# Optimization experiments

Measured on AMD Instinct MI355X. Metric: run time of the kernel, lower is better.

The kernel has to match this reference:

```python
import jax, jax.numpy as jnp
import numpy as np

NUM_HEADS = 4
NUM_GROUPS = 8
EPS = 1e-5


def group_norm(x, gamma, beta):
    B, C, H, W = x.shape
    xg = x.reshape(B, NUM_GROUPS, C // NUM_GROUPS, H, W)
    mean = xg.mean(axis=(2, 3, 4), keepdims=True)
    var = xg.var(axis=(2, 3, 4), keepdims=True)
    xn = ((xg - mean) * jax.lax.rsqrt(var + EPS)).reshape(B, C, H, W)
    return xn * gamma[None, :, None, None] + beta[None, :, None, None]


def setup_inputs() -> dict:
    key = jax.random.key(0)
    k1, k2, k3 = jax.random.split(key, 3)
    B, C, H, W = 16, 512, 32, 32
    x = jax.random.normal(k1, (B, C, H, W), dtype=jnp.float32)
    gn_gamma = jnp.ones((C,), dtype=jnp.float32)
    gn_beta = jnp.zeros((C,), dtype=jnp.float32)
    w_qkv = jax.random.normal(k2, (3 * C, C), dtype=jnp.float32) * 0.02
    w_proj = jax.random.normal(k3, (C, C), dtype=jnp.float32) * 0.02
    b_proj = jnp.zeros((C,), dtype=jnp.float32)
    return {"x": x, "gn_gamma": gn_gamma, "gn_beta": gn_beta,
            "w_qkv": w_qkv, "w_proj": w_proj, "b_proj": b_proj}


def reference(x, gn_gamma, gn_beta, w_qkv, w_proj, b_proj):
    B, C, H, W = x.shape
    nh = NUM_HEADS
    hd = C // nh
    N = H * W

    x_norm = group_norm(x, gn_gamma, gn_beta)
    # 1x1 conv == channel matmul: (B,C,H,W) x (3C,C) -> (B,3C,H,W)
    qkv = jnp.einsum('bchw,dc->bdhw', x_norm, w_qkv)
    qkv = qkv.reshape(B, 3, nh, hd, N)
    q, k, v = qkv[:, 0], qkv[:, 1], qkv[:, 2]  # each (B, nh, hd, N)

    scale = hd ** (-0.5)
    attn = jnp.einsum('bhci,bhcj->bhij', q, k) * scale  # (B, nh, N, N)
    attn = jax.nn.softmax(attn, axis=-1)
    out = jnp.einsum('bhij,bhcj->bhci', attn, v)  # (B, nh, hd, N)
    out = out.reshape(B, C, H, W)

    proj = jnp.einsum('bchw,dc->bdhw', out, w_proj) + b_proj[None, :, None, None]
    return x + proj
```

## Files before the change

### kernel.cpp

```cpp
#include <hip/hip_runtime.h>
#include <stdint.h>

typedef unsigned short u16;
typedef unsigned int u32;
typedef __attribute__((ext_vector_type(8))) short short8;
typedef __attribute__((ext_vector_type(4))) float f32x4;
typedef __attribute__((ext_vector_type(16))) float f32x16;
typedef __attribute__((ext_vector_type(4))) u32 u32x4;

#define BATCH 16
#define CCH   512
#define NPIX  1024
#define NGRP  8
#define CPG   64
#define NHEAD 4
#define HDIM  128

__device__ __forceinline__ u16 f2bf(float f) {
  union { float f; u32 u; } v; v.f = f;
  u32 u = v.u;
  u32 r = (u + 0x7FFFu + ((u >> 16) & 1u)) >> 16;
  return (u16)r;
}

__device__ __forceinline__ void gload16(const void* g, void* l) {
  typedef __attribute__((address_space(3))) u32 L;
  typedef __attribute__((address_space(1))) const u32 G;
  __builtin_amdgcn_global_load_lds((G*)(uintptr_t)g, (L*)(u32)(uintptr_t)l, 16, 0, 0);
}

#define CVTPK(dst, a, b) asm("v_cvt_pk_bf16_f32 %0, %1, %2" : "=v"(dst) : "v"(a), "v"(b))
#define PLSWAP(a, b) asm("v_permlane32_swap_b32 %0, %1" : "+v"(a), "+v"(b))

__device__ __forceinline__ short8 rd512(const char* base, int r, int ck, int hi) {
  int byte = ((r >> 2) * 512) +
             ((((r & 3) * 128) + ck * 32 + hi * 16) ^ (((r >> 2) & 15) << 4));
  return *reinterpret_cast<const short8*>(base + byte);
}

__device__ __forceinline__ float softmax_pack(const f32x16& s0, const f32x16& s1, short8* pf) {
  float ps[4] = {0.f, 0.f, 0.f, 0.f};
  u32 pw[16];
  #pragma unroll
  for (int u = 0; u < 8; ++u) {
    float pa = exp2f(s0[2*u]);  float pb = exp2f(s0[2*u+1]);
    float pc = exp2f(s1[2*u]);  float pd = exp2f(s1[2*u+1]);
    ps[u & 3] += (pa + pb) + (pc + pd);
    CVTPK(pw[u],     pa, pb);
    CVTPK(pw[8 + u], pc, pd);
  }
  PLSWAP(pw[0], pw[2]);  PLSWAP(pw[1], pw[3]);
  PLSWAP(pw[4], pw[6]);  PLSWAP(pw[5], pw[7]);
  PLSWAP(pw[8], pw[10]); PLSWAP(pw[9], pw[11]);
  PLSWAP(pw[12], pw[14]); PLSWAP(pw[13], pw[15]);
  #pragma unroll
  for (int f = 0; f < 4; ++f) {
    u32x4 t = {pw[f*4], pw[f*4+1], pw[f*4+2], pw[f*4+3]};
    pf[f] = __builtin_bit_cast(short8, t);
  }
  float psum = (ps[0] + ps[1]) + (ps[2] + ps[3]);
  psum += __shfl_xor(psum, 32);
  return psum;
}

__global__ void gn_stats_k(const float* __restrict__ x, float* __restrict__ part) {
  int bg = blockIdx.x >> 3, sl = blockIdx.x & 7;
  const float* p = x + (size_t)bg * (CPG * NPIX) + sl * 8192;
  float s = 0.f, ss = 0.f;
  for (int i = threadIdx.x; i < 2048; i += 256) {
    float4 v = reinterpret_cast<const float4*>(p)[i];
    s  += v.x + v.y + v.z + v.w;
    ss += v.x*v.x + v.y*v.y + v.z*v.z + v.w*v.w;
  }
  for (int o = 32; o > 0; o >>= 1) { s += __shfl_down(s, o); ss += __shfl_down(ss, o); }
  __shared__ float sh[8];
  int wid = threadIdx.x >> 6;
  if ((threadIdx.x & 63) == 0) { sh[wid*2] = s; sh[wid*2+1] = ss; }
  __syncthreads();
  if (threadIdx.x == 0) {
    part[blockIdx.x*2]   = sh[0]+sh[2]+sh[4]+sh[6];
    part[blockIdx.x*2+1] = sh[1]+sh[3]+sh[5]+sh[7];
  }
}

__global__ __launch_bounds__(256) void gn_apply_t(const float* __restrict__ x,
                                                  const float* __restrict__ gamma,
                                                  const float* __restrict__ beta,
                                                  const float* __restrict__ part,
                                                  u16* __restrict__ xnT) {
  const int p0 = blockIdx.x * 64;
  const int c0 = blockIdx.y * 64;
  const int b  = blockIdx.z;
  __shared__ float lt[64][66];

  const int bg = b * NGRP + (c0 >> 6);
  float s = 0.f, ss = 0.f;
  #pragma unroll
  for (int k2 = 0; k2 < 8; ++k2) { s += part[(bg*8 + k2)*2]; ss += part[(bg*8 + k2)*2 + 1]; }
  const float invn = 1.f / (float)(CPG * NPIX);
  const float mean = s * invn;
  const float rstd = rsqrtf(ss * invn - mean * mean + 1e-5f);

  const int t = threadIdx.x;
  #pragma unroll
  for (int pass = 0; pass < 4; ++pass) {
    int c   = c0 + (t >> 4) + pass * 16;
    int pix = p0 + (t & 15) * 4;
    float ga = gamma[c] * rstd;
    float be = beta[c] - mean * ga;
    float4 v = *reinterpret_cast<const float4*>(&x[((size_t)(b*CCH + c)) * NPIX + pix]);
    int pl = (t & 15) * 4, cl = (t >> 4) + pass * 16;
    lt[pl+0][cl] = v.x*ga + be;
    lt[pl+1][cl] = v.y*ga + be;
    lt[pl+2][cl] = v.z*ga + be;
    lt[pl+3][cl] = v.w*ga + be;
  }
  __syncthreads();
  const int pl = t >> 2, cq = (t & 3) * 16;
  u32 wbuf[8];
  #pragma unroll
  for (int e = 0; e < 8; ++e) {
    u16 lo = f2bf(lt[pl][cq + e*2]);
    u16 hi = f2bf(lt[pl][cq + e*2 + 1]);
    wbuf[e] = (u32)lo | ((u32)hi << 16);
  }
  u32* dst = (u32*)&xnT[((size_t)(b*NPIX + p0 + pl)) * CCH + c0 + cq];
  #pragma unroll
  for (int e = 0; e < 8; ++e) dst[e] = wbuf[e];
}

__global__ void f2bf_all(const float* __restrict__ wqkv, const float* __restrict__ wproj,
                         u16* __restrict__ wq, u16* __restrict__ wp, float qs) {
  int i = blockIdx.x * 256 + threadIdx.x;
  float4 v; u16* dst; float sc = 1.f;
  if (i < 196608) {
    v = reinterpret_cast<const float4*>(wqkv)[i];
    if (i < 65536) sc = qs;
    dst = wq + (size_t)i * 4;
  } else {
    v = reinterpret_cast<const float4*>(wproj)[i - 196608];
    dst = wp + (size_t)(i - 196608) * 4;
  }
  u32 lo = (u32)f2bf(v.x*sc) | ((u32)f2bf(v.y*sc) << 16);
  u32 hi = (u32)f2bf(v.z*sc) | ((u32)f2bf(v.w*sc) << 16);
  *reinterpret_cast<uint2*>(dst) = make_uint2(lo, hi);
}

__global__ __launch_bounds__(256, 2) void gemm_qkv(const u16* __restrict__ xnT,
                                                   const u16* __restrict__ wq_bf,
                                                   u16* __restrict__ outQ,
                                                   u16* __restrict__ outK,
                                                   u16* __restrict__ outV) {
  __shared__ __align__(16) char smem[65536];

  const int id = blockIdx.x;
  const int wg = (id & 7) * 192 + (id >> 3);
  const bool mode0 = (wg < 1024);
  int rt, ct;
  if (mode0) { rt = wg >> 3; ct = wg & 7; }
  else       { int w1 = wg - 1024; rt = w1 & 3; ct = w1 >> 2; }

  const char* Ab = mode0 ? (const char*)xnT + (size_t)rt * 131072
                         : (const char*)wq_bf + (size_t)(8 + rt) * 131072;
  const char* Bb = mode0 ? (const char*)wq_bf + (size_t)ct * 131072
                         : (const char*)xnT + (size_t)ct * 131072;

  const int t = threadIdx.x;
  const int lane = t & 63, w = t >> 6;
  const int q = lane & 31, hi = lane >> 5;
  const int rh = (w >> 1) * 64, ch = (w & 1) * 64;

  int soff[4];
  #pragma unroll
  for (int i = 0; i < 4; ++i) {
    int p = w*4096 + i*1024 + lane*16;
    int lrow = p >> 9, off = p & 511;
    int loff = off ^ ((lrow & 15) << 4);
    soff[i] = (lrow*4 + (loff >> 7)) * 1024 + (loff & 127);
  }

  #pragma unroll
  for (int i = 0; i < 4; ++i) {
    gload16(Ab + soff[i], smem +         w*4096 + i*1024);
    gload16(Bb + soff[i], smem + 16384 + w*4096 + i*1024);
  }

  f32x16 acc[2][2] = {};

  for (int kt = 0; kt < 8; ++kt) {
    asm volatile("s_waitcnt vmcnt(0)" ::: "memory");
    __syncthreads();
    const char* cur = smem + (kt & 1) * 32768;
    if (kt + 1 < 8) {
      char* nxt = smem + ((kt + 1) & 1) * 32768;
      #pragma unroll
      for (int i = 0; i < 4; ++i) {
        gload16(Ab + (kt+1)*128 + soff[i], nxt +         w*4096 + i*1024);
        gload16(Bb + (kt+1)*128 + soff[i], nxt + 16384 + w*4096 + i*1024);
      }
    }
    __builtin_amdgcn_s_setprio(1);
    #pragma unroll
    for (int ck = 0; ck < 4; ++ck) {
      short8 af0 = rd512(cur,         rh + q,      ck, hi);
      short8 af1 = rd512(cur,         rh + 32 + q, ck, hi);
      short8 bf0 = rd512(cur + 16384, ch + q,      ck, hi);
      short8 bf1 = rd512(cur + 16384, ch + 32 + q, ck, hi);
      acc[0][0] = __builtin_amdgcn_mfma_f32_32x32x16_bf16(af0, bf0, acc[0][0], 0, 0, 0);
      acc[0][1] = __builtin_amdgcn_mfma_f32_32x32x16_bf16(af0, bf1, acc[0][1], 0, 0, 0);
      acc[1][0] = __builtin_amdgcn_mfma_f32_32x32x16_bf16(af1, bf0, acc[1][0], 0, 0, 0);
      acc[1][1] = __builtin_amdgcn_mfma_f32_32x32x16_bf16(af1, bf1, acc[1][1], 0, 0, 0);
    }
    __builtin_amdgcn_s_setprio(0);
  }

  __syncthreads();
  u16* Dt = (u16*)smem;
  #pragma unroll
  for (int r = 0; r < 16; ++r) {
    int ar = (r & 3) + 8*(r >> 2) + 4*hi;
    Dt[(rh +      ar) * 136 + ch +      q] = f2bf(acc[0][0][r]);
    Dt[(rh +      ar) * 136 + ch + 32 + q] = f2bf(acc[0][1][r]);
    Dt[(rh + 32 + ar) * 136 + ch +      q] = f2bf(acc[1][0][r]);
    Dt[(rh + 32 + ar) * 136 + ch + 32 + q] = f2bf(acc[1][1][r]);
  }
  __syncthreads();

  const int rl = t >> 1, hoff = (t & 1) * 64;
  uint4 buf[8];
  const uint4* s4 = reinterpret_cast<const uint4*>(&Dt[rl*136 + hoff]);
  #pragma unroll
  for (int e = 0; e < 8; ++e) buf[e] = s4[e];

  u16* gdst;
  if (mode0) {
    const int tok0 = rt * 128;
    const int b = tok0 >> 10, pix0 = tok0 & 1023;
    const int h = ct & 3;
    u16* base = (ct >= 4) ? outK : outQ;
    gdst = base + ((size_t)((b*NHEAD + h)) * NPIX + pix0 + rl) * HDIM + hoff;
  } else {
    const int m0 = rt * 128, tok0 = ct * 128;
    const int b = tok0 >> 10, pix0 = tok0 & 1023;
    gdst = outV + ((size_t)(b*CCH + m0 + rl)) * NPIX + pix0 + hoff;
  }
  uint4* g4 = reinterpret_cast<uint4*>(gdst);
  #pragma unroll
  for (int e = 0; e < 8; ++e) g4[e] = buf[e];
}

__global__ __launch_bounds__(256, 2) void gemm_proj(const u16* __restrict__ wp_bf,
                                                    const u16* __restrict__ attnO,
                                                    const float* __restrict__ xres,
                                                    const float* __restrict__ bias,
                                                    float* __restrict__ outF) {
  __shared__ __align__(16) char smem[65536];

  const int id = blockIdx.x;
  const int wg = (id & 7) * 64 + (id >> 3);
  const int rt = wg & 3, ct = wg >> 2;

  const char* Ab = (const char*)wp_bf + (size_t)rt * 131072;
  const char* Bb = (const char*)attnO + (size_t)ct * 131072;

  const int t = threadIdx.x;
  const int lane = t & 63, w = t >> 6;
  const int q = lane & 31, hi = lane >> 5;
  const int rh = (w >> 1) * 64, ch = (w & 1) * 64;

  int soff[4];
  #pragma unroll
  for (int i = 0; i < 4; ++i) {
    int p = w*4096 + i*1024 + lane*16;
    int lrow = p >> 9, off = p & 511;
    int loff = off ^ ((lrow & 15) << 4);
    soff[i] = (lrow*4 + (loff >> 7)) * 1024 + (loff & 127);
  }

  #pragma unroll
  for (int i = 0; i < 4; ++i) {
    gload16(Ab + soff[i], smem +         w*4096 + i*1024);
    gload16(Bb + soff[i], smem + 16384 + w*4096 + i*1024);
  }

  f32x16 acc[2][2] = {};

  for (int kt = 0; kt < 8; ++kt) {
    asm volatile("s_waitcnt vmcnt(0)" ::: "memory");
    __syncthreads();
    const char* cur = smem + (kt & 1) * 32768;
    if (kt + 1 < 8) {
      char* nxt = smem + ((kt + 1) & 1) * 32768;
      #pragma unroll
      for (int i = 0; i < 4; ++i) {
        gload16(Ab + (kt+1)*128 + soff[i], nxt +         w*4096 + i*1024);
        gload16(Bb + (kt+1)*128 + soff[i], nxt + 16384 + w*4096 + i*1024);
      }
    }
    __builtin_amdgcn_s_setprio(1);
    #pragma unroll
    for (int ck = 0; ck < 4; ++ck) {
      short8 af0 = rd512(cur,         rh + q,      ck, hi);
      short8 af1 = rd512(cur,         rh + 32 + q, ck, hi);
      short8 bf0 = rd512(cur + 16384, ch + q,      ck, hi);
      short8 bf1 = rd512(cur + 16384, ch + 32 + q, ck, hi);
      acc[0][0] = __builtin_amdgcn_mfma_f32_32x32x16_bf16(af0, bf0, acc[0][0], 0, 0, 0);
      acc[0][1] = __builtin_amdgcn_mfma_f32_32x32x16_bf16(af0, bf1, acc[0][1], 0, 0, 0);
      acc[1][0] = __builtin_amdgcn_mfma_f32_32x32x16_bf16(af1, bf0, acc[1][0], 0, 0, 0);
      acc[1][1] = __builtin_amdgcn_mfma_f32_32x32x16_bf16(af1, bf1, acc[1][1], 0, 0, 0);
    }
    __builtin_amdgcn_s_setprio(0);
  }

  const int m0 = rt * 128, tok0 = ct * 128;
  const int b = tok0 >> 10, pix0 = tok0 & 1023;
  #pragma unroll
  for (int r = 0; r < 16; ++r) {
    int ar = (r & 3) + 8*(r >> 2) + 4*hi;
    int m0r = m0 + rh + ar, m1r = m0 + rh + 32 + ar;
    size_t o00 = ((size_t)(b*CCH + m0r)) * NPIX + pix0 + ch + q;
    size_t o01 = o00 + 32;
    size_t o10 = ((size_t)(b*CCH + m1r)) * NPIX + pix0 + ch + q;
    size_t o11 = o10 + 32;
    outF[o00] = xres[o00] + acc[0][0][r] + bias[m0r];
    outF[o01] = xres[o01] + acc[0][1][r] + bias[m0r];
    outF[o10] = xres[o10] + acc[1][0][r] + bias[m1r];
    outF[o11] = xres[o11] + acc[1][1][r] + bias[m1r];
  }
}

__global__ __launch_bounds__(256, 2) void attn_k(const u16* __restrict__ Qt,
                                                 const u16* __restrict__ Kt,
                                                 const u16* __restrict__ Vb,
                                                 u16* __restrict__ attnO) {
  int id = blockIdx.x;
  int swz = (id & 7) * 64 + (id >> 3);
  const int qt = swz & 7;
  const int h  = (swz >> 3) & 3;
  const int b  = swz >> 5;
  const int bh = b * NHEAD + h;

  __shared__ __align__(16) char smem[65536];

  const int t = threadIdx.x;
  const int lane = t & 63, w = t >> 6;
  const int q = lane & 31, hi = lane >> 5;

  const u16*  Qb    = Qt + ((size_t)bh * NPIX + qt*128 + w*32 + q) * HDIM;
  const char* Kbase = (const char*)(Kt + (size_t)bh * NPIX * HDIM);
  const char* Vbase = (const char*)(Vb + ((size_t)b*CCH + h*HDIM) * NPIX);

  short8 qf[8];
  #pragma unroll
  for (int ck = 0; ck < 8; ++ck)
    qf[ck] = *reinterpret_cast<const short8*>(&Qb[ck*16 + hi*8]);

  int koff[4], voff[4];
  #pragma unroll
  for (int i = 0; i < 4; ++i) {
    int d = w*4096 + i*1024 + lane*16;
    int r = d >> 8, cb = d & 255;
    int col = cb ^ ((r & 15) << 4);
    koff[i] = r*256 + col;
    int half = col >> 7, kvb = col & 127;
    voff[i] = (2*r + half)*2048 + kvb;
  }

  const int ksw = (q & 15) << 4;
  const int vsw = (q >> 1) << 4;

  f32x16 of[4] = {};
  float l_run = 0.f;
  short8 pf[4];

  #pragma unroll
  for (int i = 0; i < 4; ++i)
    gload16(Kbase + koff[i],                  smem +         w*4096 + i*1024);
  #pragma unroll
  for (int i = 0; i < 4; ++i)
    gload16(Kbase + (size_t)64*256 + koff[i], smem + 16384 + w*4096 + i*1024);
  #pragma unroll
  for (int i = 0; i < 4; ++i)
    gload16(Vbase + voff[i],                  smem + 32768 + w*4096 + i*1024);
  asm volatile("s_waitcnt vmcnt(0)" ::: "memory");
  __syncthreads();

  {
    f32x16 sn[2] = {};
    #pragma unroll
    for (int ck = 0; ck < 8; ++ck) {
      const short8 kf0 = *reinterpret_cast<const short8*>(smem + q*256      + ((ck*32 + hi*16) ^ ksw));
      const short8 kf1 = *reinterpret_cast<const short8*>(smem + (32+q)*256 + ((ck*32 + hi*16) ^ ksw));
      sn[0] = __builtin_amdgcn_mfma_f32_32x32x16_bf16(kf0, qf[ck], sn[0], 0, 0, 0);
      sn[1] = __builtin_amdgcn_mfma_f32_32x32x16_bf16(kf1, qf[ck], sn[1], 0, 0, 0);
    }
    l_run += softmax_pack(sn[0], sn[1], pf);
  }

  for (int tt = 0; tt < 16; ++tt) {
    asm volatile("s_waitcnt vmcnt(4)" ::: "memory");
    __builtin_amdgcn_s_barrier();

    const char* kcur = smem + (((tt+1) & 1) << 14);
    const char* vcur = smem + 32768 + ((tt & 1) << 14);

    if (tt + 2 < 16) {
      char* kdst = smem + ((tt & 1) << 14);
      #pragma unroll
      for (int i = 0; i < 4; ++i)
        gload16(Kbase + (size_t)(tt+2)*64*256 + koff[i], kdst + w*4096 + i*1024);
    }
    if (tt + 1 < 16) {
      char* vdst = smem + 32768 + (((tt+1) & 1) << 14);
      #pragma unroll
      for (int i = 0; i < 4; ++i)
        gload16(Vbase + (size_t)(tt+1)*128 + voff[i], vdst + w*4096 + i*1024);
    }

    f32x16 sn[2] = {};
    __builtin_amdgcn_s_setprio(1);
    if (tt + 1 < 16) {
      #pragma unroll
      for (int ck = 0; ck < 8; ++ck) {
        const short8 kf0 = *reinterpret_cast<const short8*>(kcur + q*256      + ((ck*32 + hi*16) ^ ksw));
        const short8 kf1 = *reinterpret_cast<const short8*>(kcur + (32+q)*256 + ((ck*32 + hi*16) ^ ksw));
        sn[0] = __builtin_amdgcn_mfma_f32_32x32x16_bf16(kf0, qf[ck], sn[0], 0, 0, 0);
        sn[1] = __builtin_amdgcn_mfma_f32_32x32x16_bf16(kf1, qf[ck], sn[1], 0, 0, 0);
      }
    }
    __builtin_amdgcn_s_setprio(0);

    if (tt < 14)       asm volatile("s_waitcnt vmcnt(8)" ::: "memory");
    else if (tt == 14) asm volatile("s_waitcnt vmcnt(4)" ::: "memory");
    else               asm volatile("s_waitcnt vmcnt(0)" ::: "memory");
    __builtin_amdgcn_s_barrier();

    __builtin_amdgcn_s_setprio(1);
    #pragma unroll
    for (int cg = 0; cg < 4; ++cg) {
      const char* vrow = vcur + (cg*16 + (q >> 1))*256;
      const int hb = (q & 1) << 7;
      #pragma unroll
      for (int kc = 0; kc < 4; ++kc)
        of[cg] = __builtin_amdgcn_mfma_f32_32x32x16_bf16(
            *reinterpret_cast<const short8*>(vrow + ((hb + kc*32 + hi*16) ^ vsw)),
            pf[kc], of[cg], 0, 0, 0);
    }
    __builtin_amdgcn_s_setprio(0);

    if (tt + 1 < 16)
      l_run += softmax_pack(sn[0], sn[1], pf);
  }

  float inv = 1.f / l_run;
  u16* orow = attnO + ((size_t)(b*NPIX + qt*128 + w*32 + q)) * CCH + h*HDIM;
  #pragma unroll
  for (int cg = 0; cg < 4; ++cg) {
    #pragma unroll
    for (int u = 0; u < 8; ++u) {
      int c = cg*32 + ((2*u) & 3) + 8*(u >> 1) + 4*hi;
      u32 pk = (u32)f2bf(of[cg][2*u] * inv) | ((u32)f2bf(of[cg][2*u+1] * inv) << 16);
      *reinterpret_cast<u32*>(&orow[c]) = pk;
    }
  }
}

extern "C" void kernel_launch(void* const* d_in, const int* in_sizes, int n_in,
                              void* d_out, int out_size, void* d_ws, size_t ws_size,
                              hipStream_t stream) {
  const float* x     = (const float*)d_in[0];
  const float* gamma = (const float*)d_in[1];
  const float* beta  = (const float*)d_in[2];
  const float* wqkv  = (const float*)d_in[3];
  const float* wproj = (const float*)d_in[4];
  const float* bproj = (const float*)d_in[5];
  float* out = (float*)d_out;

  char* ws = (char*)d_ws;
  float* part   = (float*)ws;
  u16*   xnT    = (u16*)(ws + 8192);
  u16*   wq_bf  = (u16*)(ws + 8192 + (16u<<20));
  u16*   wp_bf  = (u16*)((char*)wq_bf + 1572864);
  u16*   Qt     = (u16*)((char*)wp_bf + 524288);
  u16*   Kt     = (u16*)((char*)Qt + (16u<<20));
  u16*   Vb     = (u16*)((char*)Kt + (16u<<20));
  u16*   attnO  = (u16*)((char*)Vb + (16u<<20));

  const float qs = 0.08838834764831845f * 1.44269504088896f;

  gn_stats_k<<<dim3(1024), dim3(256), 0, stream>>>(x, part);
  gn_apply_t<<<dim3(16, 8, BATCH), dim3(256), 0, stream>>>(x, gamma, beta, part, xnT);
  f2bf_all<<<dim3(1024), dim3(256), 0, stream>>>(wqkv, wproj, wq_bf, wp_bf, qs);

  gemm_qkv<<<dim3(1536), dim3(256), 0, stream>>>(xnT, wq_bf, Qt, Kt, Vb);

  attn_k<<<dim3(512), dim3(256), 0, stream>>>(Qt, Kt, Vb, attnO);

  gemm_proj<<<dim3(512), dim3(256), 0, stream>>>(wp_bf, attnO, x, bproj, out);
}
```

Measured before the change: 122.5 us.

## Split KV tile across wave pairs with two query subtiles per wave in attention

```diff
diff --git a/kernel.cpp b/kernel.cpp
--- a/kernel.cpp
+++ b/kernel.cpp
@@ -38,29 +38,23 @@
   return *reinterpret_cast<const short8*>(base + byte);
 }
 
-__device__ __forceinline__ float softmax_pack(const f32x16& s0, const f32x16& s1, short8* pf) {
-  float ps[4] = {0.f, 0.f, 0.f, 0.f};
-  u32 pw[16];
+__device__ __forceinline__ float softmax_pack32(const f32x16& sn, short8* pf) {
+  float ps = 0.f;
+  u32 pw[8];
   #pragma unroll
   for (int u = 0; u < 8; ++u) {
-    float pa = exp2f(s0[2*u]);  float pb = exp2f(s0[2*u+1]);
-    float pc = exp2f(s1[2*u]);  float pd = exp2f(s1[2*u+1]);
-    ps[u & 3] += (pa + pb) + (pc + pd);
-    CVTPK(pw[u],     pa, pb);
-    CVTPK(pw[8 + u], pc, pd);
-  }
-  PLSWAP(pw[0], pw[2]);  PLSWAP(pw[1], pw[3]);
-  PLSWAP(pw[4], pw[6]);  PLSWAP(pw[5], pw[7]);
-  PLSWAP(pw[8], pw[10]); PLSWAP(pw[9], pw[11]);
-  PLSWAP(pw[12], pw[14]); PLSWAP(pw[13], pw[15]);
-  #pragma unroll
-  for (int f = 0; f < 4; ++f) {
-    u32x4 t = {pw[f*4], pw[f*4+1], pw[f*4+2], pw[f*4+3]};
-    pf[f] = __builtin_bit_cast(short8, t);
-  }
-  float psum = (ps[0] + ps[1]) + (ps[2] + ps[3]);
-  psum += __shfl_xor(psum, 32);
-  return psum;
+    float pa = exp2f(sn[2*u]);
+    float pb = exp2f(sn[2*u+1]);
+    ps += pa + pb;
+    CVTPK(pw[u], pa, pb);
+  }
+  PLSWAP(pw[0], pw[2]); PLSWAP(pw[1], pw[3]);
+  PLSWAP(pw[4], pw[6]); PLSWAP(pw[5], pw[7]);
+  u32x4 t0 = {pw[0], pw[1], pw[2], pw[3]};
+  u32x4 t1 = {pw[4], pw[5], pw[6], pw[7]};
+  pf[0] = __builtin_bit_cast(short8, t0);
+  pf[1] = __builtin_bit_cast(short8, t1);
+  return ps;
 }
 
 __global__ void gn_stats_k(const float* __restrict__ x, float* __restrict__ part) {
@@ -340,20 +334,23 @@
   const int b  = swz >> 5;
   const int bh = b * NHEAD + h;
 
-  __shared__ __align__(16) char smem[65536];
+  __shared__ __align__(16) char smem[66048];
 
   const int t = threadIdx.x;
   const int lane = t & 63, w = t >> 6;
   const int q = lane & 31, hi = lane >> 5;
-
-  const u16*  Qb    = Qt + ((size_t)bh * NPIX + qt*128 + w*32 + q) * HDIM;
+  const int qsub = w & 1, kvh = w >> 1;
+
+  const u16*  Qb    = Qt + ((size_t)bh * NPIX + qt*128 + qsub*64 + q) * HDIM;
   const char* Kbase = (const char*)(Kt + (size_t)bh * NPIX * HDIM);
   const char* Vbase = (const char*)(Vb + ((size_t)b*CCH + h*HDIM) * NPIX);
 
-  short8 qf[8];
-  #pragma unroll
-  for (int ck = 0; ck < 8; ++ck)
-    qf[ck] = *reinterpret_cast<const short8*>(&Qb[ck*16 + hi*8]);
+  short8 qf0[8], qf1[8];
+  #pragma unroll
+  for (int ck = 0; ck < 8; ++ck) {
+    qf0[ck] = *reinterpret_cast<const short8*>(&Qb[ck*16 + hi*8]);
+    qf1[ck] = *reinterpret_cast<const short8*>(&Qb[(size_t)32*HDIM + ck*16 + hi*8]);
+  }
 
   int koff[4], voff[4];
   #pragma unroll
@@ -366,74 +363,53 @@
     voff[i] = (2*r + half)*2048 + kvb;
   }
 
-  const int ksw = (q & 15) << 4;
-  const int vsw = (q >> 1) << 4;
-
-  f32x16 of[4] = {};
-  float l_run = 0.f;
-  short8 pf[4];
+  const int ksw  = (q & 15) << 4;
+  const int vsw  = (q >> 1) << 4;
+  const int krow = (kvh*32 + q) * 256;
+  const int vkvb = kvh * 64;
+
+  f32x16 of0[4] = {};
+  f32x16 of1[4] = {};
+  float l0 = 0.f, l1 = 0.f;
 
   #pragma unroll
   for (int i = 0; i < 4; ++i)
-    gload16(Kbase + koff[i],                  smem +         w*4096 + i*1024);
+    gload16(Kbase + koff[i], smem + w*4096 + i*1024);
   #pragma unroll
   for (int i = 0; i < 4; ++i)
-    gload16(Kbase + (size_t)64*256 + koff[i], smem + 16384 + w*4096 + i*1024);
-  #pragma unroll
-  for (int i = 0; i < 4; ++i)
-    gload16(Vbase + voff[i],                  smem + 32768 + w*4096 + i*1024);
-  asm volatile("s_waitcnt vmcnt(0)" ::: "memory");
-  __syncthreads();
-
-  {
-    f32x16 sn[2] = {};
+    gload16(Vbase + voff[i], smem + 32768 + w*4096 + i*1024);
+
+  for (int tt = 0; tt < 16; ++tt) {
+    asm volatile("s_waitcnt vmcnt(0)" ::: "memory");
+    __builtin_amdgcn_s_barrier();
+
+    const char* kcur = smem + ((tt & 1) << 14);
+    const char* vcur = smem + 32768 + ((tt & 1) << 14);
+
+    if (tt + 1 < 16) {
+      char* kd = smem + (((tt+1) & 1) << 14);
+      char* vd = smem + 32768 + (((tt+1) & 1) << 14);
+      #pragma unroll
+      for (int i = 0; i < 4; ++i)
+        gload16(Kbase + (size_t)(tt+1)*16384 + koff[i], kd + w*4096 + i*1024);
+      #pragma unroll
+      for (int i = 0; i < 4; ++i)
+        gload16(Vbase + (size_t)(tt+1)*128 + voff[i], vd + w*4096 + i*1024);
+    }
+
+    f32x16 sn0 = {}, sn1 = {};
+    __builtin_amdgcn_s_setprio(1);
     #pragma unroll
     for (int ck = 0; ck < 8; ++ck) {
-      const short8 kf0 = *reinterpret_cast<const short8*>(smem + q*256      + ((ck*32 + hi*16) ^ ksw));
-      const short8 kf1 = *reinterpret_cast<const short8*>(smem + (32+q)*256 + ((ck*32 + hi*16) ^ ksw));
-      sn[0] = __builtin_amdgcn_mfma_f32_32x32x16_bf16(kf0, qf[ck], sn[0], 0, 0, 0);
-      sn[1] = __builtin_amdgcn_mfma_f32_32x32x16_bf16(kf1, qf[ck], sn[1], 0, 0, 0);
-    }
-    l_run += softmax_pack(sn[0], sn[1], pf);
-  }
-
-  for (int tt = 0; tt < 16; ++tt) {
-    asm volatile("s_waitcnt vmcnt(4)" ::: "memory");
-    __builtin_amdgcn_s_barrier();
-
-    const char* kcur = smem + (((tt+1) & 1) << 14);
-    const char* vcur = smem + 32768 + ((tt & 1) << 14);
-
-    if (tt + 2 < 16) {
-      char* kdst = smem + ((tt & 1) << 14);
-      #pragma unroll
-      for (int i = 0; i < 4; ++i)
-        gload16(Kbase + (size_t)(tt+2)*64*256 + koff[i], kdst + w*4096 + i*1024);
-    }
-    if (tt + 1 < 16) {
-      char* vdst = smem + 32768 + (((tt+1) & 1) << 14);
-      #pragma unroll
-      for (int i = 0; i < 4; ++i)
-        gload16(Vbase + (size_t)(tt+1)*128 + voff[i], vdst + w*4096 + i*1024);
-    }
-
-    f32x16 sn[2] = {};
-    __builtin_amdgcn_s_setprio(1);
-    if (tt + 1 < 16) {
-      #pragma unroll
-      for (int ck = 0; ck < 8; ++ck) {
-        const short8 kf0 = *reinterpret_cast<const short8*>(kcur + q*256      + ((ck*32 + hi*16) ^ ksw));
-        const short8 kf1 = *reinterpret_cast<const short8*>(kcur + (32+q)*256 + ((ck*32 + hi*16) ^ ksw));
-        sn[0] = __builtin_amdgcn_mfma_f32_32x32x16_bf16(kf0, qf[ck], sn[0], 0, 0, 0);
-        sn[1] = __builtin_amdgcn_mfma_f32_32x32x16_bf16(kf1, qf[ck], sn[1], 0, 0, 0);
-      }
+      const short8 kf = *reinterpret_cast<const short8*>(kcur + krow + ((ck*32 + hi*16) ^ ksw));
+      sn0 = __builtin_amdgcn_mfma_f32_32x32x16_bf16(kf, qf0[ck], sn0, 0, 0, 0);
+      sn1 = __builtin_amdgcn_mfma_f32_32x32x16_bf16(kf, qf1[ck], sn1, 0, 0, 0);
     }
     __builtin_amdgcn_s_setprio(0);
 
-    if (tt < 14)       asm volatile("s_waitcnt vmcnt(8)" ::: "memory");
-    else if (tt == 14) asm volatile("s_waitcnt vmcnt(4)" ::: "memory");
-    else               asm volatile("s_waitcnt vmcnt(0)" ::: "memory");
-    __builtin_amdgcn_s_barrier();
+    short8 pfa[2], pfb[2];
+    l0 += softmax_pack32(sn0, pfa);
+    l1 += softmax_pack32(sn1, pfb);
 
     __builtin_amdgcn_s_setprio(1);
     #pragma unroll
@@ -441,26 +417,54 @@
       const char* vrow = vcur + (cg*16 + (q >> 1))*256;
       const int hb = (q & 1) << 7;
       #pragma unroll
-      for (int kc = 0; kc < 4; ++kc)
-        of[cg] = __builtin_amdgcn_mfma_f32_32x32x16_bf16(
-            *reinterpret_cast<const short8*>(vrow + ((hb + kc*32 + hi*16) ^ vsw)),
-            pf[kc], of[cg], 0, 0, 0);
+      for (int kc = 0; kc < 2; ++kc) {
+        const short8 vf = *reinterpret_cast<const short8*>(
+            vrow + ((hb + vkvb + kc*32 + hi*16) ^ vsw));
+        of0[cg] = __builtin_amdgcn_mfma_f32_32x32x16_bf16(vf, pfa[kc], of0[cg], 0, 0, 0);
+        of1[cg] = __builtin_amdgcn_mfma_f32_32x32x16_bf16(vf, pfb[kc], of1[cg], 0, 0, 0);
+      }
     }
     __builtin_amdgcn_s_setprio(0);
-
-    if (tt + 1 < 16)
-      l_run += softmax_pack(sn[0], sn[1], pf);
-  }
-
-  float inv = 1.f / l_run;
-  u16* orow = attnO + ((size_t)(b*NPIX + qt*128 + w*32 + q)) * CCH + h*HDIM;
-  #pragma unroll
-  for (int cg = 0; cg < 4; ++cg) {
+  }
+
+  __syncthreads();
+  float* exf = (float*)smem;
+  float* exl = (float*)(smem + 65536);
+
+  l0 += __shfl_xor(l0, 32);
+  l1 += __shfl_xor(l1, 32);
+
+  if (kvh == 1) {
     #pragma unroll
-    for (int u = 0; u < 8; ++u) {
-      int c = cg*32 + ((2*u) & 3) + 8*(u >> 1) + 4*hi;
-      u32 pk = (u32)f2bf(of[cg][2*u] * inv) | ((u32)f2bf(of[cg][2*u+1] * inv) << 16);
-      *reinterpret_cast<u32*>(&orow[c]) = pk;
+    for (int cg = 0; cg < 4; ++cg)
+      #pragma unroll
+      for (int r = 0; r < 16; ++r) {
+        exf[qsub*8192 + cg*2048 + r*128 +      lane] = of0[cg][r];
+        exf[qsub*8192 + cg*2048 + r*128 + 64 + lane] = of1[cg][r];
+      }
+    if (lane < 32) {
+      exl[qsub*64 +      q] = l0;
+      exl[qsub*64 + 32 + q] = l1;
+    }
+  }
+  __syncthreads();
+  if (kvh == 0) {
+    const float inv0 = 1.f / (l0 + exl[qsub*64 + q]);
+    const float inv1 = 1.f / (l1 + exl[qsub*64 + 32 + q]);
+    u16* orow0 = attnO + ((size_t)(b*NPIX + qt*128 + qsub*64 + q)) * CCH + h*HDIM;
+    u16* orow1 = orow0 + (size_t)32 * CCH;
+    #pragma unroll
+    for (int cg = 0; cg < 4; ++cg) {
+      #pragma unroll
+      for (int u = 0; u < 8; ++u) {
+        int c = cg*32 + ((2*u) & 3) + 8*(u >> 1) + 4*hi;
+        float a0 = (of0[cg][2*u]   + exf[qsub*8192 + cg*2048 + (2*u)*128 +      lane]) * inv0;
+        float a1 = (of0[cg][2*u+1] + exf[qsub*8192 + cg*2048 + (2*u+1)*128 +    lane]) * inv0;
+        float b0 = (of1[cg][2*u]   + exf[qsub*8192 + cg*2048 + (2*u)*128 + 64 + lane]) * inv1;
+        float b1 = (of1[cg][2*u+1] + exf[qsub*8192 + cg*2048 + (2*u+1)*128 + 64 + lane]) * inv1;
+        *reinterpret_cast<u32*>(&orow0[c]) = (u32)f2bf(a0) | ((u32)f2bf(a1) << 16);
+        *reinterpret_cast<u32*>(&orow1[c]) = (u32)f2bf(b0) | ((u32)f2bf(b1) << 16);
+      }
     }
   }
 }
```

New measurement: 142.0 us. 15.9% more time.

## Switch attention Q/K/V and probabilities to FP8 MFMA

Applied to the files above, without the earlier changes.

```diff
diff --git a/kernel.cpp b/kernel.cpp
--- a/kernel.cpp
+++ b/kernel.cpp
@@ -1,8 +1,10 @@
 #include <hip/hip_runtime.h>
 #include <stdint.h>
 
+typedef unsigned char u8;
 typedef unsigned short u16;
 typedef unsigned int u32;
+typedef long long i64;
 typedef __attribute__((ext_vector_type(8))) short short8;
 typedef __attribute__((ext_vector_type(4))) float f32x4;
 typedef __attribute__((ext_vector_type(16))) float f32x16;
@@ -22,6 +24,14 @@
   u32 r = (u + 0x7FFFu + ((u >> 16) & 1u)) >> 16;
   return (u16)r;
 }
+__device__ __forceinline__ u8 f2fp8(float f) {
+  return (u8)(__builtin_amdgcn_cvt_pk_fp8_f32(f, 0.f, 0, false) & 0xff);
+}
+__device__ __forceinline__ u32 pack4_fp8(float a, float b, float c, float d) {
+  u32 w = (u32)__builtin_amdgcn_cvt_pk_fp8_f32(a, b, 0, false);
+  w = (u32)__builtin_amdgcn_cvt_pk_fp8_f32(c, d, (int)w, true);
+  return w;
+}
 
 __device__ __forceinline__ void gload16(const void* g, void* l) {
   typedef __attribute__((address_space(3))) u32 L;
@@ -29,38 +39,12 @@
   __builtin_amdgcn_global_load_lds((G*)(uintptr_t)g, (L*)(u32)(uintptr_t)l, 16, 0, 0);
 }
 
-#define CVTPK(dst, a, b) asm("v_cvt_pk_bf16_f32 %0, %1, %2" : "=v"(dst) : "v"(a), "v"(b))
 #define PLSWAP(a, b) asm("v_permlane32_swap_b32 %0, %1" : "+v"(a), "+v"(b))
 
 __device__ __forceinline__ short8 rd512(const char* base, int r, int ck, int hi) {
   int byte = ((r >> 2) * 512) +
              ((((r & 3) * 128) + ck * 32 + hi * 16) ^ (((r >> 2) & 15) << 4));
   return *reinterpret_cast<const short8*>(base + byte);
-}
-
-__device__ __forceinline__ float softmax_pack(const f32x16& s0, const f32x16& s1, short8* pf) {
-  float ps[4] = {0.f, 0.f, 0.f, 0.f};
-  u32 pw[16];
-  #pragma unroll
-  for (int u = 0; u < 8; ++u) {
-    float pa = exp2f(s0[2*u]);  float pb = exp2f(s0[2*u+1]);
-    float pc = exp2f(s1[2*u]);  float pd = exp2f(s1[2*u+1]);
-    ps[u & 3] += (pa + pb) + (pc + pd);
-    CVTPK(pw[u],     pa, pb);
-    CVTPK(pw[8 + u], pc, pd);
-  }
-  PLSWAP(pw[0], pw[2]);  PLSWAP(pw[1], pw[3]);
-  PLSWAP(pw[4], pw[6]);  PLSWAP(pw[5], pw[7]);
-  PLSWAP(pw[8], pw[10]); PLSWAP(pw[9], pw[11]);
-  PLSWAP(pw[12], pw[14]); PLSWAP(pw[13], pw[15]);
-  #pragma unroll
-  for (int f = 0; f < 4; ++f) {
-    u32x4 t = {pw[f*4], pw[f*4+1], pw[f*4+2], pw[f*4+3]};
-    pf[f] = __builtin_bit_cast(short8, t);
-  }
-  float psum = (ps[0] + ps[1]) + (ps[2] + ps[3]);
-  psum += __shfl_xor(psum, 32);
-  return psum;
 }
 
 __global__ void gn_stats_k(const float* __restrict__ x, float* __restrict__ part) {
@@ -130,27 +114,26 @@
 }
 
 __global__ void f2bf_all(const float* __restrict__ wqkv, const float* __restrict__ wproj,
-                         u16* __restrict__ wq, u16* __restrict__ wp, float qs) {
+                         u16* __restrict__ wq, u16* __restrict__ wp) {
   int i = blockIdx.x * 256 + threadIdx.x;
-  float4 v; u16* dst; float sc = 1.f;
+  float4 v; u16* dst;
   if (i < 196608) {
     v = reinterpret_cast<const float4*>(wqkv)[i];
-    if (i < 65536) sc = qs;
     dst = wq + (size_t)i * 4;
   } else {
     v = reinterpret_cast<const float4*>(wproj)[i - 196608];
     dst = wp + (size_t)(i - 196608) * 4;
   }
-  u32 lo = (u32)f2bf(v.x*sc) | ((u32)f2bf(v.y*sc) << 16);
-  u32 hi = (u32)f2bf(v.z*sc) | ((u32)f2bf(v.w*sc) << 16);
+  u32 lo = (u32)f2bf(v.x) | ((u32)f2bf(v.y) << 16);
+  u32 hi = (u32)f2bf(v.z) | ((u32)f2bf(v.w) << 16);
   *reinterpret_cast<uint2*>(dst) = make_uint2(lo, hi);
 }
 
 __global__ __launch_bounds__(256, 2) void gemm_qkv(const u16* __restrict__ xnT,
                                                    const u16* __restrict__ wq_bf,
-                                                   u16* __restrict__ outQ,
-                                                   u16* __restrict__ outK,
-                                                   u16* __restrict__ outV) {
+                                                   u8* __restrict__ outQ,
+                                                   u8* __restrict__ outK,
+                                                   u8* __restrict__ outV) {
   __shared__ __align__(16) char smem[65536];
 
   const int id = blockIdx.x;
@@ -215,29 +198,29 @@
   }
 
   __syncthreads();
-  u16* Dt = (u16*)smem;
+  u8* Dt = (u8*)smem;
   #pragma unroll
   for (int r = 0; r < 16; ++r) {
     int ar = (r & 3) + 8*(r >> 2) + 4*hi;
-    Dt[(rh +      ar) * 136 + ch +      q] = f2bf(acc[0][0][r]);
-    Dt[(rh +      ar) * 136 + ch + 32 + q] = f2bf(acc[0][1][r]);
-    Dt[(rh + 32 + ar) * 136 + ch +      q] = f2bf(acc[1][0][r]);
-    Dt[(rh + 32 + ar) * 136 + ch + 32 + q] = f2bf(acc[1][1][r]);
+    Dt[(rh +      ar) * 144 + ch +      q] = f2fp8(acc[0][0][r]);
+    Dt[(rh +      ar) * 144 + ch + 32 + q] = f2fp8(acc[0][1][r]);
+    Dt[(rh + 32 + ar) * 144 + ch +      q] = f2fp8(acc[1][0][r]);
+    Dt[(rh + 32 + ar) * 144 + ch + 32 + q] = f2fp8(acc[1][1][r]);
   }
   __syncthreads();
 
   const int rl = t >> 1, hoff = (t & 1) * 64;
-  uint4 buf[8];
-  const uint4* s4 = reinterpret_cast<const uint4*>(&Dt[rl*136 + hoff]);
-  #pragma unroll
-  for (int e = 0; e < 8; ++e) buf[e] = s4[e];
-
-  u16* gdst;
+  uint4 buf[4];
+  const uint4* s4 = reinterpret_cast<const uint4*>(&Dt[rl*144 + hoff]);
+  #pragma unroll
+  for (int e = 0; e < 4; ++e) buf[e] = s4[e];
+
+  u8* gdst;
   if (mode0) {
     const int tok0 = rt * 128;
     const int b = tok0 >> 10, pix0 = tok0 & 1023;
     const int h = ct & 3;
-    u16* base = (ct >= 4) ? outK : outQ;
+    u8* base = (ct >= 4) ? outK : outQ;
     gdst = base + ((size_t)((b*NHEAD + h)) * NPIX + pix0 + rl) * HDIM + hoff;
   } else {
     const int m0 = rt * 128, tok0 = ct * 128;
@@ -246,7 +229,7 @@
   }
   uint4* g4 = reinterpret_cast<uint4*>(gdst);
   #pragma unroll
-  for (int e = 0; e < 8; ++e) g4[e] = buf[e];
+  for (int e = 0; e < 4; ++e) g4[e] = buf[e];
 }
 
 __global__ __launch_bounds__(256, 2) void gemm_proj(const u16* __restrict__ wp_bf,
@@ -329,9 +312,9 @@
   }
 }
 
-__global__ __launch_bounds__(256, 2) void attn_k(const u16* __restrict__ Qt,
-                                                 const u16* __restrict__ Kt,
-                                                 const u16* __restrict__ Vb,
+__global__ __launch_bounds__(256, 2) void attn_k(const u8* __restrict__ Qt,
+                                                 const u8* __restrict__ Kt,
+                                                 const u8* __restrict__ Vb,
                                                  u16* __restrict__ attnO) {
   int id = blockIdx.x;
   int swz = (id & 7) * 64 + (id >> 3);
@@ -340,116 +323,151 @@
   const int b  = swz >> 5;
   const int bh = b * NHEAD + h;
 
-  __shared__ __align__(16) char smem[65536];
+  __shared__ __align__(16) char smem[32768];
 
   const int t = threadIdx.x;
   const int lane = t & 63, w = t >> 6;
   const int q = lane & 31, hi = lane >> 5;
 
-  const u16*  Qb    = Qt + ((size_t)bh * NPIX + qt*128 + w*32 + q) * HDIM;
-  const char* Kbase = (const char*)(Kt + (size_t)bh * NPIX * HDIM);
-  const char* Vbase = (const char*)(Vb + ((size_t)b*CCH + h*HDIM) * NPIX);
-
-  short8 qf[8];
+  const u8*   Qb    = Qt + ((size_t)bh * NPIX + qt*128 + w*32 + q) * HDIM;
+  const char* Kbase = (const char*)Kt + (size_t)bh * NPIX * HDIM;
+  const char* Vbase = (const char*)Vb + ((size_t)b*CCH + h*HDIM) * NPIX;
+
+  i64 qf[8];
   #pragma unroll
   for (int ck = 0; ck < 8; ++ck)
-    qf[ck] = *reinterpret_cast<const short8*>(&Qb[ck*16 + hi*8]);
-
-  int koff[4], voff[4];
-  #pragma unroll
-  for (int i = 0; i < 4; ++i) {
-    int d = w*4096 + i*1024 + lane*16;
-    int r = d >> 8, cb = d & 255;
-    int col = cb ^ ((r & 15) << 4);
-    koff[i] = r*256 + col;
-    int half = col >> 7, kvb = col & 127;
-    voff[i] = (2*r + half)*2048 + kvb;
-  }
-
-  const int ksw = (q & 15) << 4;
-  const int vsw = (q >> 1) << 4;
+    qf[ck] = *reinterpret_cast<const i64*>(Qb + ck*16 + hi*8);
+
+  int koff[2], voff[2];
+  #pragma unroll
+  for (int i = 0; i < 2; ++i) {
+    int d = i*4096 + w*1024 + lane*16;
+    int r = d >> 7, x = d & 127;
+    koff[i] = r*128 + (x ^ ((r & 15) << 3));
+    int vc = 2*r + (x >> 6);
+    voff[i] = vc*1024 + ((x & 63) ^ ((r & 7) << 3));
+  }
+
+  const int ksw = (q & 15) << 3;
 
   f32x16 of[4] = {};
   float l_run = 0.f;
-  short8 pf[4];
-
-  #pragma unroll
-  for (int i = 0; i < 4; ++i)
-    gload16(Kbase + koff[i],                  smem +         w*4096 + i*1024);
-  #pragma unroll
-  for (int i = 0; i < 4; ++i)
-    gload16(Kbase + (size_t)64*256 + koff[i], smem + 16384 + w*4096 + i*1024);
-  #pragma unroll
-  for (int i = 0; i < 4; ++i)
-    gload16(Vbase + voff[i],                  smem + 32768 + w*4096 + i*1024);
+  i64 pf[4];
+  const float qs2 = 0.08838834764831845f * 1.44269504088896f;
+
+  #pragma unroll
+  for (int i = 0; i < 2; ++i)
+    gload16(Kbase + koff[i],        smem +        i*4096 + w*1024);
+  #pragma unroll
+  for (int i = 0; i < 2; ++i)
+    gload16(Kbase + 8192 + koff[i], smem + 8192 + i*4096 + w*1024);
+  #pragma unroll
+  for (int i = 0; i < 2; ++i)
+    gload16(Vbase + voff[i],        smem + 16384 + i*4096 + w*1024);
   asm volatile("s_waitcnt vmcnt(0)" ::: "memory");
   __syncthreads();
 
   {
-    f32x16 sn[2] = {};
+    f32x16 sn0 = {}, sn1 = {};
     #pragma unroll
     for (int ck = 0; ck < 8; ++ck) {
-      const short8 kf0 = *reinterpret_cast<const short8*>(smem + q*256      + ((ck*32 + hi*16) ^ ksw));
-      const short8 kf1 = *reinterpret_cast<const short8*>(smem + (32+q)*256 + ((ck*32 + hi*16) ^ ksw));
-      sn[0] = __builtin_amdgcn_mfma_f32_32x32x16_bf16(kf0, qf[ck], sn[0], 0, 0, 0);
-      sn[1] = __builtin_amdgcn_mfma_f32_32x32x16_bf16(kf1, qf[ck], sn[1], 0, 0, 0);
-    }
-    l_run += softmax_pack(sn[0], sn[1], pf);
+      const i64 kf0 = *reinterpret_cast<const i64*>(smem + q*128      + ((ck*16 + hi*8) ^ ksw));
+      const i64 kf1 = *reinterpret_cast<const i64*>(smem + (32+q)*128 + ((ck*16 + hi*8) ^ ksw));
+      sn0 = __builtin_amdgcn_mfma_f32_32x32x16_fp8_fp8(kf0, qf[ck], sn0, 0, 0, 0);
+      sn1 = __builtin_amdgcn_mfma_f32_32x32x16_fp8_fp8(kf1, qf[ck], sn1, 0, 0, 0);
+    }
+    float ps = 0.f;
+    float p[16];
+    #pragma unroll
+    for (int g = 0; g < 2; ++g) {
+      const f32x16& sn = g ? sn1 : sn0;
+      #pragma unroll
+      for (int r = 0; r < 16; ++r) { p[r] = exp2f(sn[r] * qs2); ps += p[r]; }
+      u32 pkl0 = pack4_fp8(p[0], p[1], p[2], p[3]);
+      u32 pkh0 = pack4_fp8(p[4], p[5], p[6], p[7]);
+      u32 pkl1 = pack4_fp8(p[8], p[9], p[10], p[11]);
+      u32 pkh1 = pack4_fp8(p[12], p[13], p[14], p[15]);
+      PLSWAP(pkl0, pkh0);
+      PLSWAP(pkl1, pkh1);
+      pf[g*2]   = (i64)(((unsigned long long)pkh0 << 32) | pkl0);
+      pf[g*2+1] = (i64)(((unsigned long long)pkh1 << 32) | pkl1);
+    }
+    ps += __shfl_xor(ps, 32);
+    l_run += ps;
   }
 
   for (int tt = 0; tt < 16; ++tt) {
-    asm volatile("s_waitcnt vmcnt(4)" ::: "memory");
+    asm volatile("s_waitcnt vmcnt(2)" ::: "memory");
     __builtin_amdgcn_s_barrier();
 
-    const char* kcur = smem + (((tt+1) & 1) << 14);
-    const char* vcur = smem + 32768 + ((tt & 1) << 14);
+    const char* kcur = smem + (((tt+1) & 1) << 13);
+    const char* vcur = smem + 16384 + ((tt & 1) << 13);
 
     if (tt + 2 < 16) {
-      char* kdst = smem + ((tt & 1) << 14);
-      #pragma unroll
-      for (int i = 0; i < 4; ++i)
-        gload16(Kbase + (size_t)(tt+2)*64*256 + koff[i], kdst + w*4096 + i*1024);
+      char* kd = smem + ((tt & 1) << 13);
+      #pragma unroll
+      for (int i = 0; i < 2; ++i)
+        gload16(Kbase + (size_t)(tt+2)*8192 + koff[i], kd + i*4096 + w*1024);
     }
     if (tt + 1 < 16) {
-      char* vdst = smem + 32768 + (((tt+1) & 1) << 14);
-      #pragma unroll
-      for (int i = 0; i < 4; ++i)
-        gload16(Vbase + (size_t)(tt+1)*128 + voff[i], vdst + w*4096 + i*1024);
-    }
-
-    f32x16 sn[2] = {};
+      char* vd = smem + 16384 + (((tt+1) & 1) << 13);
+      #pragma unroll
+      for (int i = 0; i < 2; ++i)
+        gload16(Vbase + (size_t)(tt+1)*64 + voff[i], vd + i*4096 + w*1024);
+    }
+
+    f32x16 sn0 = {}, sn1 = {};
     __builtin_amdgcn_s_setprio(1);
     if (tt + 1 < 16) {
       #pragma unroll
       for (int ck = 0; ck < 8; ++ck) {
-        const short8 kf0 = *reinterpret_cast<const short8*>(kcur + q*256      + ((ck*32 + hi*16) ^ ksw));
-        const short8 kf1 = *reinterpret_cast<const short8*>(kcur + (32+q)*256 + ((ck*32 + hi*16) ^ ksw));
-        sn[0] = __builtin_amdgcn_mfma_f32_32x32x16_bf16(kf0, qf[ck], sn[0], 0, 0, 0);
-        sn[1] = __builtin_amdgcn_mfma_f32_32x32x16_bf16(kf1, qf[ck], sn[1], 0, 0, 0);
+        const i64 kf0 = *reinterpret_cast<const i64*>(kcur + q*128      + ((ck*16 + hi*8) ^ ksw));
+        const i64 kf1 = *reinterpret_cast<const i64*>(kcur + (32+q)*128 + ((ck*16 + hi*8) ^ ksw));
+        sn0 = __builtin_amdgcn_mfma_f32_32x32x16_fp8_fp8(kf0, qf[ck], sn0, 0, 0, 0);
+        sn1 = __builtin_amdgcn_mfma_f32_32x32x16_fp8_fp8(kf1, qf[ck], sn1, 0, 0, 0);
       }
     }
     __builtin_amdgcn_s_setprio(0);
 
-    if (tt < 14)       asm volatile("s_waitcnt vmcnt(8)" ::: "memory");
-    else if (tt == 14) asm volatile("s_waitcnt vmcnt(4)" ::: "memory");
+    if (tt < 14)       asm volatile("s_waitcnt vmcnt(4)" ::: "memory");
+    else if (tt == 14) asm volatile("s_waitcnt vmcnt(2)" ::: "memory");
     else               asm volatile("s_waitcnt vmcnt(0)" ::: "memory");
     __builtin_amdgcn_s_barrier();
 
     __builtin_amdgcn_s_setprio(1);
     #pragma unroll
     for (int cg = 0; cg < 4; ++cg) {
-      const char* vrow = vcur + (cg*16 + (q >> 1))*256;
-      const int hb = (q & 1) << 7;
-      #pragma unroll
-      for (int kc = 0; kc < 4; ++kc)
-        of[cg] = __builtin_amdgcn_mfma_f32_32x32x16_bf16(
-            *reinterpret_cast<const short8*>(vrow + ((hb + kc*32 + hi*16) ^ vsw)),
-            pf[kc], of[cg], 0, 0, 0);
+      const int c = cg*32 + q;
+      const char* vrow = vcur + (c >> 1)*128 + (c & 1)*64;
+      const int vsw = ((c >> 1) & 7) << 3;
+      #pragma unroll
+      for (int kc = 0; kc < 4; ++kc) {
+        const i64 vf = *reinterpret_cast<const i64*>(vrow + ((kc*16 + hi*8) ^ vsw));
+        of[cg] = __builtin_amdgcn_mfma_f32_32x32x16_fp8_fp8(vf, pf[kc], of[cg], 0, 0, 0);
+      }
     }
     __builtin_amdgcn_s_setprio(0);
 
-    if (tt + 1 < 16)
-      l_run += softmax_pack(sn[0], sn[1], pf);
+    if (tt + 1 < 16) {
+      float ps = 0.f;
+      float p[16];
+      #pragma unroll
+      for (int g = 0; g < 2; ++g) {
+        const f32x16& sn = g ? sn1 : sn0;
+        #pragma unroll
+        for (int r = 0; r < 16; ++r) { p[r] = exp2f(sn[r] * qs2); ps += p[r]; }
+        u32 pkl0 = pack4_fp8(p[0], p[1], p[2], p[3]);
+        u32 pkh0 = pack4_fp8(p[4], p[5], p[6], p[7]);
+        u32 pkl1 = pack4_fp8(p[8], p[9], p[10], p[11]);
+        u32 pkh1 = pack4_fp8(p[12], p[13], p[14], p[15]);
+        PLSWAP(pkl0, pkh0);
+        PLSWAP(pkl1, pkh1);
+        pf[g*2]   = (i64)(((unsigned long long)pkh0 << 32) | pkl0);
+        pf[g*2+1] = (i64)(((unsigned long long)pkh1 << 32) | pkl1);
+      }
+      ps += __shfl_xor(ps, 32);
+      l_run += ps;
+    }
   }
 
   float inv = 1.f / l_run;
@@ -481,16 +499,14 @@
   u16*   xnT    = (u16*)(ws + 8192);
   u16*   wq_bf  = (u16*)(ws + 8192 + (16u<<20));
   u16*   wp_bf  = (u16*)((char*)wq_bf + 1572864);
-  u16*   Qt     = (u16*)((char*)wp_bf + 524288);
-  u16*   Kt     = (u16*)((char*)Qt + (16u<<20));
-  u16*   Vb     = (u16*)((char*)Kt + (16u<<20));
-  u16*   attnO  = (u16*)((char*)Vb + (16u<<20));
-
-  const float qs = 0.08838834764831845f * 1.44269504088896f;
+  u8*    Qt     = (u8*)((char*)wp_bf + 524288);
+  u8*    Kt     = (u8*)((char*)Qt + (8u<<20));
+  u8*    Vb     = (u8*)((char*)Kt + (8u<<20));
+  u16*   attnO  = (u16*)((char*)Vb + (8u<<20));
 
   gn_stats_k<<<dim3(1024), dim3(256), 0, stream>>>(x, part);
   gn_apply_t<<<dim3(16, 8, BATCH), dim3(256), 0, stream>>>(x, gamma, beta, part, xnT);
-  f2bf_all<<<dim3(1024), dim3(256), 0, stream>>>(wqkv, wproj, wq_bf, wp_bf, qs);
+  f2bf_all<<<dim3(1024), dim3(256), 0, stream>>>(wqkv, wproj, wq_bf, wp_bf);
 
   gemm_qkv<<<dim3(1536), dim3(256), 0, stream>>>(xnT, wq_bf, Qt, Kt, Vb);
 
```

After: 113.0 us. 1.08x faster.
